# Optimization experiments

Measured on AMD Instinct MI355X. Metric: run time of the kernel, lower is better.

The kernel has to match this reference:

```python
import jax, jax.numpy as jnp
import numpy as np

BANDS, D_MODEL, NCLASS = 200, 256, 17
EXPAND, D_STATE, D_CONV, HEADDIM = 2, 128, 4, 64
D_INNER = EXPAND * D_MODEL            # 512
NHEADS = D_INNER // HEADDIM           # 8
D_IN_PROJ = 2 * D_INNER + 2 * D_STATE + NHEADS  # 1288 (ngroups=1)
CHUNK = 256


def _segsum(a):
    # a: (..., Q) -> (..., Q, Q); out[i,j] = sum_{k=j+1..i} a[k] (i>=j), else -inf
    q = a.shape[-1]
    cs = jnp.cumsum(a, axis=-1)
    d = cs[..., :, None] - cs[..., None, :]
    mask = jnp.tril(jnp.ones((q, q), dtype=bool))
    return jnp.where(mask, d, -jnp.inf)


def _ssd(Xd, Adt, B, C, Q):
    # Chunked SSD (exact selective-scan). Xd=(b,l,h,p) is x*dt, Adt=(b,l,h) is A*dt, B,C=(b,l,n)
    b, l, h, p = Xd.shape
    n = B.shape[-1]
    c = l // Q
    Xc = Xd.reshape(b, c, Q, h, p)
    Bc = B.reshape(b, c, Q, n)
    Cc = C.reshape(b, c, Q, n)
    Ac = Adt.reshape(b, c, Q, h).transpose(0, 3, 1, 2)      # (b,h,c,Q)
    Acs = jnp.cumsum(Ac, axis=-1)
    Lm = jnp.exp(_segsum(Ac))                                # (b,h,c,Q,Q) lower-tri decay
    Yd = jnp.einsum('bcqn,bckn,bhcqk,bckhp->bcqhp', Cc, Bc, Lm, Xc)
    decay_states = jnp.exp(Acs[..., -1:] - Acs)              # (b,h,c,Q)
    states = jnp.einsum('bcqn,bhcq,bcqhp->bchpn', Bc, decay_states, Xc)
    chunk_decay = jnp.exp(Acs[..., -1])                      # (b,h,c)
    def step(carry, inp):
        s, d = inp
        return carry * d[..., None, None] + s, carry
    _, prev = jax.lax.scan(step, jnp.zeros((b, h, p, n), Xd.dtype),
                           (states.transpose(1, 0, 2, 3, 4), chunk_decay.transpose(2, 0, 1)))
    prev = prev.transpose(1, 0, 2, 3, 4)                     # (b,c,h,p,n) state entering each chunk
    Yo = jnp.einsum('bcqn,bchpn,bhcq->bcqhp', Cc, prev, jnp.exp(Acs))
    return (Yd + Yo).reshape(b, l, h, p)


def setup_inputs() -> dict:
    ks = jax.random.split(jax.random.key(0), 8)
    b, l = 16, 1024
    dt0 = jnp.exp(jax.random.uniform(ks[1], (NHEADS,), minval=np.log(1e-3), maxval=np.log(0.1)))
    return {
        'x': jax.random.normal(ks[0], (b, l, BANDS), jnp.float32),
        'w_inp': jax.random.normal(ks[2], (BANDS, D_MODEL)) * 0.05,
        'b_inp': jnp.zeros((D_MODEL,)),
        'w_in': jax.random.normal(ks[3], (D_MODEL, D_IN_PROJ)) * 0.05,
        'conv_w': jax.random.normal(ks[4], (D_CONV, D_INNER + 2 * D_STATE)) * 0.2,
        'conv_b': jnp.zeros((D_INNER + 2 * D_STATE,)),
        'dt_bias': jnp.log(jnp.expm1(dt0)),                 # inverse softplus
        'A_log': jnp.log(jnp.arange(1, NHEADS + 1, dtype=jnp.float32)),
        'D': jnp.ones((NHEADS,)),
        'rms_w': jnp.ones((D_INNER,)),
        'w_out': jax.random.normal(ks[5], (D_INNER, D_MODEL)) * 0.04,
        'ln_g': jnp.ones((D_MODEL,)),
        'ln_b': jnp.zeros((D_MODEL,)),
        'w_cls': jax.random.normal(ks[6], (D_MODEL, NCLASS)) * 0.06,
        'b_cls': jnp.zeros((NCLASS,)),
    }


def reference(x, w_inp, b_inp, w_in, conv_w, conv_b, dt_bias, A_log, D,
              rms_w, w_out, ln_g, ln_b, w_cls, b_cls):
    b, l, _ = x.shape
    u = x @ w_inp + b_inp                                    # input_proj: (b,l,d_model)
    zxbcdt = u @ w_in                                        # (b,l,1288)
    z, xBC, dt = jnp.split(zxbcdt, [D_INNER, 2 * D_INNER + 2 * D_STATE], axis=-1)
    dt = jax.nn.softplus(dt + dt_bias)                       # (b,l,nheads)
    # causal depthwise conv1d + SiLU
    xBC = jax.lax.conv_general_dilated(
        xBC, conv_w[:, None, :], (1,), [(D_CONV - 1, 0)],
        dimension_numbers=('NWC', 'WIO', 'NWC'),
        feature_group_count=D_INNER + 2 * D_STATE) + conv_b
    xBC = jax.nn.silu(xBC)
    xh, B, C = jnp.split(xBC, [D_INNER, D_INNER + D_STATE], axis=-1)
    xh = xh.reshape(b, l, NHEADS, HEADDIM)
    A = -jnp.exp(A_log)                                      # (nheads,)
    y = _ssd(xh * dt[..., None], dt * A, B, C, CHUNK)        # (b,l,h,p)
    y = y + xh * D[None, None, :, None]                      # D skip
    y = y.reshape(b, l, D_INNER)
    # gated RMSNorm (norm_before_gate=False): rmsnorm(y * silu(z)) * w
    y = y * jax.nn.silu(z)
    y = y * jax.lax.rsqrt(jnp.mean(y * y, axis=-1, keepdims=True) + 1e-5) * rms_w
    y = y @ w_out                                            # out_proj (no bias)
    # classifier: LayerNorm -> Dropout(eval=identity) -> Linear
    mu = jnp.mean(y, axis=-1, keepdims=True)
    var = jnp.mean((y - mu) ** 2, axis=-1, keepdims=True)
    y = (y - mu) * jax.lax.rsqrt(var + 1e-5) * ln_g + ln_b
    return y @ w_cls + b_cls
```

## Files before the change

kernel.cpp:

```cpp
#include <hip/hip_runtime.h>
#include <math.h>

#define ROWS   16384L
#define LSEQ   1024
#define NB     16
#define DM     256
#define DPROJ  1288
#define XBCW   768
#define DIN    512
#define DSTATE 128
#define NH     8
#define HD     64
#define QLEN   256
#define NCHUNK 4
#define NCLS   17

typedef __attribute__((ext_vector_type(8))) short s16x8;
typedef __attribute__((ext_vector_type(4))) float f32x4;

#define GLOAD_LDS16(gsrc, ldst) \
  __builtin_amdgcn_global_load_lds((const __attribute__((address_space(1))) void*)(gsrc), \
      (__attribute__((address_space(3))) void*)(ldst), 16, 0, 0)

constexpr long O_GBF  = 0;
constexpr long O_ZX   = O_GBF + ROWS*DM;
constexpr long O_XBC  = O_ZX  + ROWS*DPROJ;
constexpr long O_DT   = O_XBC + ROWS*XBCW;
constexpr long O_ACS  = O_DT  + ROWS*NH;
constexpr long O_Y    = O_ACS + 131072;
constexpr long O_ST   = O_Y   + ROWS*DIN;
constexpr long O_Y2   = O_ST  + 4194304;
constexpr long O_XBF  = O_XBC;
constexpr long O_BBF  = O_XBC + 4200000;
constexpr long O_CBF  = O_XBC + 5300000;
constexpr long O_BT   = O_XBC + 6400000;
constexpr long O_YBF  = O_Y;
constexpr long O_XPBF = O_Y + 4300000;
constexpr long O_WCT  = O_Y + 6200000;
constexpr long O_WOUTT= O_Y + 6400000;
constexpr long O_WDT  = O_Y + 6500000;
constexpr long O_WCLST= O_Y + 6530000;
constexpr long O_WINT = O_Y + 6600000;
constexpr long O_WIPE = O_Y + 6800000;

__device__ inline unsigned short f2bf(float f) {
  union { float f; unsigned u; } v; v.f = f;
  unsigned r = v.u + 0x7FFFu + ((v.u >> 16) & 1u);
  return (unsigned short)(r >> 16);
}
__device__ inline float bf2f(unsigned short s) {
  union { unsigned u; float f; } v; v.u = ((unsigned)s) << 16; return v.f;
}

__global__ __launch_bounds__(256) void prep_misc(
    const float* __restrict__ x, unsigned short* __restrict__ xp,
    const float* __restrict__ w_in, unsigned short* __restrict__ w_inT,
    const float* __restrict__ wout, unsigned short* __restrict__ woutT,
    const float* __restrict__ w_inp, const float* __restrict__ b_inp,
    unsigned short* __restrict__ we,
    float* __restrict__ Wdt, float* __restrict__ bdt,
    const float* __restrict__ wcls, float* __restrict__ wclsT)
{
  int bid = blockIdx.x;
  int tid = threadIdx.x;
  if (bid < 3584) {
    long idx = (long)bid * 256 + tid;
    int q = (int)(idx % 56);
    long row = idx / 56;
    ushort4 o = {0, 0, 0, 0};
    if (q < 50) {
      float4 v = *(const float4*)&x[row * 200 + q * 4];
      o.x = f2bf(v.x); o.y = f2bf(v.y); o.z = f2bf(v.z); o.w = f2bf(v.w);
    } else if (q == 50) {
      o.x = 0x3F80;
    }
    *(ushort4*)&xp[row * 224 + q * 4] = o;
  } else if (bid < 4872) {
    long i = (long)(bid - 3584) * 256 + tid;
    int k = (int)(i & 255);
    long n = i >> 8;
    w_inT[i] = f2bf(w_in[(long)k * DPROJ + n]);
  } else if (bid < 5384) {
    long i = (long)(bid - 4872) * 256 + tid;
    int k = (int)(i & 511);
    long n = i >> 9;
    woutT[i] = f2bf(wout[(long)k * DM + n]);
  } else if (bid < 5608) {
    int i = (bid - 5384) * 256 + tid;
    int k = i >> 8, j = i & 255;
    float v = 0.f;
    if (k < 200)       v = w_inp[(long)k * 256 + j];
    else if (k == 200) v = b_inp[j];
    we[i] = f2bf(v);
  } else if (bid < 5659) {
    int k = (bid - 5608) * 4 + (tid >> 6);
    if (k > 200) return;
    int lane = tid & 63;
    int j0 = lane * 4;
    float4 xv = (k < 200) ? *(const float4*)&w_inp[(long)k * 256 + j0]
                          : *(const float4*)&b_inp[j0];
    float a0 = 0.f, a1 = 0.f, a2 = 0.f, a3 = 0.f, a4 = 0.f, a5 = 0.f, a6 = 0.f, a7 = 0.f;
    float xd[4] = {xv.x, xv.y, xv.z, xv.w};
#pragma unroll
    for (int d = 0; d < 4; ++d) {
      const float* wr = &w_in[(long)(j0 + d) * DPROJ + 1280];
      float4 wa = *(const float4*)wr;
      float4 wb = *(const float4*)(wr + 4);
      a0 = fmaf(xd[d], wa.x, a0); a1 = fmaf(xd[d], wa.y, a1);
      a2 = fmaf(xd[d], wa.z, a2); a3 = fmaf(xd[d], wa.w, a3);
      a4 = fmaf(xd[d], wb.x, a4); a5 = fmaf(xd[d], wb.y, a5);
      a6 = fmaf(xd[d], wb.z, a6); a7 = fmaf(xd[d], wb.w, a7);
    }
#pragma unroll
    for (int off = 32; off; off >>= 1) {
      a0 += __shfl_xor(a0, off); a1 += __shfl_xor(a1, off);
      a2 += __shfl_xor(a2, off); a3 += __shfl_xor(a3, off);
      a4 += __shfl_xor(a4, off); a5 += __shfl_xor(a5, off);
      a6 += __shfl_xor(a6, off); a7 += __shfl_xor(a7, off);
    }
    float o = a0;
    if (lane == 1) o = a1; if (lane == 2) o = a2; if (lane == 3) o = a3;
    if (lane == 4) o = a4; if (lane == 5) o = a5; if (lane == 6) o = a6;
    if (lane == 7) o = a7;
    if (lane < 8) {
      if (k < 200) Wdt[k * 8 + lane] = o;
      else         bdt[lane] = o;
    }
  } else {
    int i = (bid - 5659) * 256 + tid;
    if (i < NCLS * 256) {
      int j = i >> 8, k = i & 255;
      wclsT[i] = wcls[(long)k * NCLS + j];
    }
  }
}

__global__ __launch_bounds__(256) void gemm_bf16(
    const unsigned short* __restrict__ A, const unsigned short* __restrict__ BT,
    float* __restrict__ C, unsigned short* __restrict__ Cb,
    const float* __restrict__ bias, int M, int N, int K)
{
  __shared__ __align__(16) unsigned short As[128 * 32];
  __shared__ __align__(16) unsigned short Bs[128 * 32];
  const int tid = threadIdx.x;
  const int m0 = blockIdx.y * 128, n0 = blockIdx.x * 128;
  const int lane = tid & 63, wv = tid >> 6;
  const int wr = (wv >> 1) * 64, wc = (wv & 1) * 64;
  f32x4 acc[4][4];
#pragma unroll
  for (int i = 0; i < 4; ++i)
#pragma unroll
    for (int j = 0; j < 4; ++j) acc[i][j] = (f32x4){0.f, 0.f, 0.f, 0.f};

  for (int k0 = 0; k0 < K; k0 += 32) {
    __syncthreads();
#pragma unroll
    for (int s = 0; s < 2; ++s) {
      int idx = (tid + 256 * s) * 8;
      int r = idx >> 5, kk = idx & 31;
      GLOAD_LDS16(&A[(long)(m0 + r) * K + k0 + kk], &As[idx]);
    }
#pragma unroll
    for (int s = 0; s < 2; ++s) {
      int idx = (tid + 256 * s) * 8;
      int n = idx >> 5, kk = idx & 31;
      int srcn = (n0 + n < N) ? (n0 + n) : 0;
      GLOAD_LDS16(&BT[(long)srcn * K + k0 + kk], &Bs[idx]);
    }
    __syncthreads();
    s16x8 af[4], bf[4];
#pragma unroll
    for (int i = 0; i < 4; ++i)
      af[i] = *(const s16x8*)&As[(wr + i * 16 + (lane & 15)) * 32 + (lane >> 4) * 8];
#pragma unroll
    for (int j = 0; j < 4; ++j)
      bf[j] = *(const s16x8*)&Bs[(wc + j * 16 + (lane & 15)) * 32 + (lane >> 4) * 8];
#pragma unroll
    for (int i = 0; i < 4; ++i)
#pragma unroll
      for (int j = 0; j < 4; ++j)
        acc[i][j] = __builtin_amdgcn_mfma_f32_16x16x32_bf16(af[i], bf[j], acc[i][j], 0, 0, 0);
  }
  const int cr = (lane >> 4) * 4, cc = lane & 15;
#pragma unroll
  for (int i = 0; i < 4; ++i)
#pragma unroll
    for (int j = 0; j < 4; ++j) {
      int col = n0 + wc + j * 16 + cc;
      if (col < N) {
        long rowb = (long)(m0 + wr + i * 16 + cr);
        float bv = bias ? bias[col] : 0.f;
#pragma unroll
        for (int r = 0; r < 4; ++r) {
          float v = acc[i][j][r] + bv;
          if (C)  C[(rowb + r) * N + col] = v;
          if (Cb) Cb[(rowb + r) * (long)N + col] = f2bf(v);
        }
      }
    }
}

__global__ __launch_bounds__(256) void g_gemm_bf16(
    const unsigned short* __restrict__ Cbf, const unsigned short* __restrict__ Bbf,
    unsigned short* __restrict__ Gbf)
{
  int bc = blockIdx.z;
  unsigned short* Gout = Gbf + (long)bc * 65536;
  const int tid = threadIdx.x;
  const int m0 = blockIdx.y * 128, n0 = blockIdx.x * 128;
  if (blockIdx.x > blockIdx.y) {
    s16x8 z = {};
    for (int e = tid; e < 128 * 16; e += 256) {
      int r = e >> 4, seg = e & 15;
      *(s16x8*)&Gout[(long)(m0 + r) * 256 + n0 + seg * 8] = z;
    }
    return;
  }
  long rowbase = (long)(bc >> 2) * LSEQ + (bc & 3) * QLEN;
  const unsigned short* A  = Cbf + rowbase * 128;
  const unsigned short* BT = Bbf + rowbase * 128;
  __shared__ __align__(16) unsigned short As[128 * 32];
  __shared__ __align__(16) unsigned short Bs[128 * 32];
  const int lane = tid & 63, wv = tid >> 6;
  const int wr = (wv >> 1) * 64, wc = (wv & 1) * 64;
  f32x4 acc[4][4];
#pragma unroll
  for (int i = 0; i < 4; ++i)
#pragma unroll
    for (int j = 0; j < 4; ++j) acc[i][j] = (f32x4){0.f, 0.f, 0.f, 0.f};
  for (int k0 = 0; k0 < 128; k0 += 32) {
    __syncthreads();
#pragma unroll
    for (int s = 0; s < 2; ++s) {
      int idx = (tid + 256 * s) * 8;
      int r = idx >> 5, kk = idx & 31;
      GLOAD_LDS16(&A[(long)(m0 + r) * 128 + k0 + kk], &As[idx]);
      GLOAD_LDS16(&BT[(long)(n0 + r) * 128 + k0 + kk], &Bs[idx]);
    }
    __syncthreads();
    s16x8 af[4], bf[4];
#pragma unroll
    for (int i = 0; i < 4; ++i)
      af[i] = *(const s16x8*)&As[(wr + i * 16 + (lane & 15)) * 32 + (lane >> 4) * 8];
#pragma unroll
    for (int j = 0; j < 4; ++j)
      bf[j] = *(const s16x8*)&Bs[(wc + j * 16 + (lane & 15)) * 32 + (lane >> 4) * 8];
#pragma unroll
    for (int i = 0; i < 4; ++i)
#pragma unroll
      for (int j = 0; j < 4; ++j)
        acc[i][j] = __builtin_amdgcn_mfma_f32_16x16x32_bf16(af[i], bf[j], acc[i][j], 0, 0, 0);
  }
  const int cr = (lane >> 4) * 4, cc = lane & 15;
#pragma unroll
  for (int i = 0; i < 4; ++i)
#pragma unroll
    for (int j = 0; j < 4; ++j) {
      int col = n0 + wc + j * 16 + cc;
      int qb = m0 + wr + i * 16 + cr;
#pragma unroll
      for (int r = 0; r < 4; ++r)
        Gout[(long)(qb + r) * 256 + col] = (col <= qb + r) ? f2bf(acc[i][j][r]) : (unsigned short)0;
    }
}

__global__ __launch_bounds__(256) void conv_silu3(
    const unsigned short* __restrict__ zxb, const float* __restrict__ cw,
    const float* __restrict__ cb,
    unsigned short* __restrict__ Xbf, unsigned short* __restrict__ Bbf,
    unsigned short* __restrict__ Cbf)
{
  long idx = (long)blockIdx.x * 256 + threadIdx.x;
  if (idx >= ROWS * 192) return;
  int cq = (int)(idx % 192);
  long row = idx / 192;
  int t = (int)(row & 1023);
  int ch = cq * 4;
  float4 cbv = *(const float4*)&cb[ch];
  float a0 = cbv.x, a1 = cbv.y, a2 = cbv.z, a3 = cbv.w;
#pragma unroll
  for (int w = 0; w < 4; ++w) {
    int d = w - 3;
    if (t + d >= 0) {
      ushort4 zv = *(const ushort4*)&zxb[(row + d) * DPROJ + 512 + ch];
      float4 cwv = *(const float4*)&cw[w * XBCW + ch];
      a0 = fmaf(bf2f(zv.x), cwv.x, a0);
      a1 = fmaf(bf2f(zv.y), cwv.y, a1);
      a2 = fmaf(bf2f(zv.z), cwv.z, a2);
      a3 = fmaf(bf2f(zv.w), cwv.w, a3);
    }
  }
  ushort4 o;
  o.x = f2bf(a0 / (1.f + __expf(-a0)));
  o.y = f2bf(a1 / (1.f + __expf(-a1)));
  o.z = f2bf(a2 / (1.f + __expf(-a2)));
  o.w = f2bf(a3 / (1.f + __expf(-a3)));
  if (ch < 512)      *(ushort4*)&Xbf[row * DIN + ch] = o;
  else if (ch < 640) *(ushort4*)&Bbf[row * 128 + ch - 512] = o;
  else               *(ushort4*)&Cbf[row * 128 + ch - 640] = o;
}

__global__ __launch_bounds__(256) void dt_logits(
    const float* __restrict__ x, const float* __restrict__ Wdt,
    const float* __restrict__ bdt, const float* __restrict__ dtb,
    float* __restrict__ dtsp)
{
  __shared__ float xs[32][201];
  __shared__ float wdt_s[1600];
  long row0 = (long)blockIdx.x * 32;
  int tid = threadIdx.x;
#pragma unroll
  for (int s = 0; s < 25; ++s) {
    int e = tid + s * 256;
    int r = e / 200, c = e % 200;
    xs[r][c] = x[(row0 + r) * 200 + c];
  }
#pragma unroll
  for (int s = 0; s < 7; ++s) {
    int e = tid + s * 256;
    if (e < 1600) wdt_s[e] = Wdt[e];
  }
  __syncthreads();
  int r = tid >> 3, h = tid & 7;
  float acc = dtb[h] + bdt[h];
  for (int i = 0; i < 200; ++i)
    acc = fmaf(xs[r][i], wdt_s[i * 8 + h], acc);
  float sp = (acc > 20.f) ? acc : log1pf(__expf(acc));
  dtsp[(row0 + r) * NH + h] = sp;
}

__global__ __launch_bounds__(256) void dt_cumsum4(
    const float* __restrict__ dtsp, const float* __restrict__ alog,
    float* __restrict__ acs)
{
  int g = ((int)blockIdx.x * 256 + (int)threadIdx.x) >> 6;
  int lane = threadIdx.x & 63;
  int c = g & 3, h = (g >> 2) & 7, b = g >> 5;
  float Ah = -__expf(alog[h]);
  long rowbase = (long)b * LSEQ + c * QLEN;
  long abase = (((long)b * NH + h) * NCHUNK + c) * QLEN;
  float v[4];
#pragma unroll
  for (int j = 0; j < 4; ++j)
    v[j] = dtsp[(rowbase + lane * 4 + j) * NH + h] * Ah;
  v[1] += v[0]; v[2] += v[1]; v[3] += v[2];
  float tot = v[3];
  float run = tot;
#pragma unroll
  for (int d = 1; d < 64; d <<= 1) {
    float t = __shfl_up(run, d);
    if (lane >= d) run += t;
  }
  float excl = run - tot;
#pragma unroll
  for (int j = 0; j < 4; ++j) acs[abase + lane * 4 + j] = excl + v[j];
}

__global__ __launch_bounds__(256) void transB(const unsigned short* __restrict__ Bbf,
                                              unsigned short* __restrict__ BbfT)
{
  __shared__ unsigned short T[128][130];
  int bc = blockIdx.y, kh = blockIdx.x;
  int tid = threadIdx.x;
  long rowbase = (long)(bc >> 2) * LSEQ + (bc & 3) * QLEN + kh * 128;
  for (int e = tid; e < 128 * 128; e += 256) {
    int r = e >> 7, n = e & 127;
    T[r][n] = Bbf[(rowbase + r) * 128 + n];
  }
  __syncthreads();
  for (int e = tid; e < 128 * 128; e += 256) {
    int n = e >> 7, k = e & 127;
    BbfT[((long)bc * 128 + n) * 256 + kh * 128 + k] = T[k][n];
  }
}

__global__ __launch_bounds__(256) void yd_states7(
    const unsigned short* __restrict__ Xbf, const float* __restrict__ dtsp,
    const float* __restrict__ acs, const unsigned short* __restrict__ Gbf,
    const unsigned short* __restrict__ BbfT,
    unsigned short* __restrict__ ybf, unsigned short* __restrict__ st)
{
  int bid = blockIdx.x;
  int xcd = bid & 7, i0 = bid >> 3;
  int bc = xcd * 8 + (i0 >> 4);
  int rem = i0 & 15, h = rem >> 1, half = rem & 1;
  int c = bc & 3, b = bc >> 2;
  int bch = bc * 8 + h;

  __shared__ __align__(16) unsigned short XdT[64][264];
  __shared__ float AcsS[256], E1f[256], E2f[256], dts[256];

  const int tid = threadIdx.x;
  const int lane = tid & 63, wv = tid >> 6;
  const bool ydw = wv < 2;
  const int qb = half == 0 ? (wv == 0 ? 0 : 3) : (wv == 0 ? 1 : 2);
  const int q0 = qb * 64;
  const int n0w = half * 64 + (wv - 2) * 32;
  long rowbase = (long)b * LSEQ + c * QLEN;
  const unsigned short* Gb  = Gbf + (long)bc * 65536;
  const unsigned short* BTg = BbfT + (long)bc * 32768;

  AcsS[tid] = acs[(((long)b * NH + h) * NCHUNK + c) * QLEN + tid];
  dts[tid]  = dtsp[(rowbase + tid) * NH + h];
  __syncthreads();
  E1f[tid] = __expf(AcsS[tid] - AcsS[tid | 63]);
  E2f[tid] = __expf(AcsS[tid | 63] - AcsS[tid]);
  float rs_[4];
  rs_[0] = 1.f;
#pragma unroll
  for (int kt = 1; kt < 4; ++kt) rs_[kt] = __expf(AcsS[kt * 64 + 63] - AcsS[kt * 64 - 1]);
  __syncthreads();
  {
    int kb = wv * 64;
#pragma unroll
    for (int s = 0; s < 16; ++s) {
      int k4 = kb + s * 4;
      ushort4 pk;
      unsigned short* pp = (unsigned short*)&pk;
#pragma unroll
      for (int j = 0; j < 4; ++j) {
        int k = k4 + j;
        float v = bf2f(Xbf[(rowbase + k) * DIN + h * HD + lane]) * dts[k] * E2f[k];
        pp[j] = f2bf(v);
      }
      *(ushort4*)&XdT[lane][k4] = pk;
    }
  }
  __syncthreads();

  f32x4 accY[4][4], accS[4][2];
#pragma unroll
  for (int i = 0; i < 4; ++i)
#pragma unroll
    for (int j = 0; j < 4; ++j) accY[i][j] = (f32x4){0.f, 0.f, 0.f, 0.f};
#pragma unroll
  for (int i = 0; i < 4; ++i)
#pragma unroll
    for (int j = 0; j < 2; ++j) accS[i][j] = (f32x4){0.f, 0.f, 0.f, 0.f};

  for (int kt = 0; kt < 4; ++kt) {
    int qlo = kt * 64;
    if (ydw) {
      if (qb >= kt) {
        if (kt)
#pragma unroll
          for (int i = 0; i < 4; ++i)
#pragma unroll
            for (int j = 0; j < 4; ++j) accY[i][j] *= rs_[kt];
#pragma unroll
        for (int ks = 0; ks < 2; ++ks) {
          s16x8 bfr[4];
#pragma unroll
          for (int j = 0; j < 4; ++j)
            bfr[j] = *(const s16x8*)&XdT[j * 16 + (lane & 15)][qlo + ks * 32 + (lane >> 4) * 8];
#pragma unroll
          for (int i = 0; i < 4; ++i) {
            s16x8 a = *(const s16x8*)&Gb[(long)(q0 + i * 16 + (lane & 15)) * 256 + qlo + ks * 32 + (lane >> 4) * 8];
#pragma unroll
            for (int j = 0; j < 4; ++j)
              accY[i][j] = __builtin_amdgcn_mfma_f32_16x16x32_bf16(a, bfr[j], accY[i][j], 0, 0, 0);
          }
        }
      }
    } else {
      if (kt)
#pragma unroll
        for (int i = 0; i < 4; ++i)
#pragma unroll
          for (int j = 0; j < 2; ++j) accS[i][j] *= rs_[kt];
#pragma unroll
      for (int ks = 0; ks < 2; ++ks) {
        s16x8 afx[4];
#pragma unroll
        for (int i = 0; i < 4; ++i)
          afx[i] = *(const s16x8*)&XdT[i * 16 + (lane & 15)][qlo + ks * 32 + (lane >> 4) * 8];
#pragma unroll
        for (int j2 = 0; j2 < 2; ++j2) {
          s16x8 bt = *(const s16x8*)&BTg[(long)(n0w + j2 * 16 + (lane & 15)) * 256 + qlo + ks * 32 + (lane >> 4) * 8];
#pragma unroll
          for (int i = 0; i < 4; ++i)
            accS[i][j2] = __builtin_amdgcn_mfma_f32_16x16x32_bf16(afx[i], bt, accS[i][j2], 0, 0, 0);
        }
      }
    }
  }
  const int cr = (lane >> 4) * 4, cc = lane & 15;
  if (ydw) {
#pragma unroll
    for (int i = 0; i < 4; ++i)
#pragma unroll
      for (int j = 0; j < 4; ++j) {
        int q = q0 + i * 16 + cr;
        int p = j * 16 + cc;
#pragma unroll
        for (int r = 0; r < 4; ++r)
          ybf[(rowbase + q + r) * DIN + h * HD + p] = f2bf(accY[i][j][r] * E1f[q + r]);
      }
  } else {
#pragma unroll
    for (int i = 0; i < 4; ++i)
#pragma unroll
      for (int j2 = 0; j2 < 2; ++j2) {
        int p = i * 16 + cr;
        int n = n0w + j2 * 16 + cc;
#pragma unroll
        for (int r = 0; r < 4; ++r)
          st[(long)bch * 8192 + (long)(p + r) * 128 + n] = f2bf(accS[i][j2][r]);
      }
  }
}

__global__ void scan_states(unsigned short* __restrict__ st, const float* __restrict__ acs)
{
  long idx = (long)blockIdx.x * 256 + threadIdx.x;
  if (idx >= (long)NB * NH * 2048) return;
  long inner = idx & 2047;
  int h = (int)((idx >> 11) & 7);
  int b = (int)(idx >> 14);
  f32x4 carry = {0.f, 0.f, 0.f, 0.f};
  for (int c = 0; c < NCHUNK; ++c) {
    float dc = __expf(acs[(((long)b * NH + h) * NCHUNK + c) * QLEN + (QLEN - 1)]);
    long si = (((long)(b * NCHUNK + c) * NH + h) << 13) + inner * 4;
    ushort4 s4 = *(ushort4*)&st[si];
    f32x4 s = {bf2f(s4.x), bf2f(s4.y), bf2f(s4.z), bf2f(s4.w)};
    ushort4 o = {f2bf(carry[0]), f2bf(carry[1]), f2bf(carry[2]), f2bf(carry[3])};
    *(ushort4*)&st[si] = o;
    carry = carry * dc + s;
  }
}

__global__ __launch_bounds__(256) void yo_combine6(
    const unsigned short* __restrict__ Xbf, const unsigned short* __restrict__ Cbf,
    const unsigned short* __restrict__ prev, const float* __restrict__ acs,
    const float* __restrict__ Dp, unsigned short* __restrict__ ybf)
{
  int bid = blockIdx.x;
  int xcd = bid & 7, i0 = bid >> 3;
  int bc = xcd * 8 + (i0 >> 3), h = i0 & 7;
  int c = bc & 3, b = bc >> 2;
  int bch = bc * 8 + h;
  __shared__ float EqA[QLEN];
  const int tid = threadIdx.x;
  const int lane = tid & 63, wv = tid >> 6;
  long rowbase = (long)b * LSEQ + c * QLEN;
  EqA[tid] = __expf(acs[(((long)b * NH + h) * NCHUNK + c) * QLEN + tid]);
  __syncthreads();
  const unsigned short* Cb = Cbf + rowbase * 128;
  const unsigned short* pv = prev + (long)bch * 8192;
  f32x4 acc[4][4];
#pragma unroll
  for (int i = 0; i < 4; ++i)
#pragma unroll
    for (int j = 0; j < 4; ++j) acc[i][j] = (f32x4){0.f, 0.f, 0.f, 0.f};
#pragma unroll
  for (int ks = 0; ks < 4; ++ks) {
    int n0 = ks * 32 + (lane >> 4) * 8;
    s16x8 bf[4];
#pragma unroll
    for (int j = 0; j < 4; ++j) {
      int p = j * 16 + (lane & 15);
      bf[j] = *(const s16x8*)&pv[p * 128 + n0];
    }
#pragma unroll
    for (int i = 0; i < 4; ++i) {
      s16x8 af = *(const s16x8*)&Cb[(long)(wv * 64 + i * 16 + (lane & 15)) * 128 + n0];
#pragma unroll
      for (int j = 0; j < 4; ++j)
        acc[i][j] = __builtin_amdgcn_mfma_f32_16x16x32_bf16(af, bf[j], acc[i][j], 0, 0, 0);
    }
  }
  const int cr = (lane >> 4) * 4, cc = lane & 15;
  float Dh = Dp[h];
#pragma unroll
  for (int i = 0; i < 4; ++i)
#pragma unroll
    for (int j = 0; j < 4; ++j) {
      int q = wv * 64 + i * 16 + cr;
      int p = j * 16 + cc;
#pragma unroll
      for (int r = 0; r < 4; ++r) {
        long row = rowbase + q + r;
        long yi = row * DIN + h * HD + p;
        float xh = bf2f(Xbf[yi]);
        float pr = bf2f(ybf[yi]);
        ybf[yi] = f2bf(pr + acc[i][j][r] * EqA[q + r] + xh * Dh);
      }
    }
}

__global__ __launch_bounds__(256) void gated_rms3(
    unsigned short* __restrict__ ybf, const unsigned short* __restrict__ zxb,
    const float* __restrict__ rmsw)
{
  long row = blockIdx.x;
  int t = threadIdx.x;
  ushort2 yv = *(const ushort2*)&ybf[row * DIN + 2 * t];
  ushort2 zv = *(const ushort2*)&zxb[row * DPROJ + 2 * t];
  float z0 = bf2f(zv.x), z1 = bf2f(zv.y);
  float v0 = bf2f(yv.x) * (z0 / (1.f + __expf(-z0)));
  float v1 = bf2f(yv.y) * (z1 / (1.f + __expf(-z1)));
  float ss = v0 * v0 + v1 * v1;
#pragma unroll
  for (int off = 32; off; off >>= 1) ss += __shfl_down(ss, off);
  __shared__ float red[4];
  if ((t & 63) == 0) red[t >> 6] = ss;
  __syncthreads();
  float tot = red[0] + red[1] + red[2] + red[3];
  float scale = rsqrtf(tot * (1.f / DIN) + 1e-5f);
  ushort2 o;
  o.x = f2bf(v0 * scale * rmsw[2 * t]);
  o.y = f2bf(v1 * scale * rmsw[2 * t + 1]);
  *(ushort2*)&ybf[row * DIN + 2 * t] = o;
}

__global__ __launch_bounds__(256) void ln_cls2(
    const unsigned short* __restrict__ y2b, const float* __restrict__ g,
    const float* __restrict__ bb, const float* __restrict__ wclsT,
    const float* __restrict__ bcls, float* __restrict__ out)
{
  long row = (long)blockIdx.x * 4 + (threadIdx.x >> 6);
  int lane = threadIdx.x & 63;
  ushort4 yv = *(const ushort4*)&y2b[row * DM + lane * 4];
  float v0 = bf2f(yv.x), v1 = bf2f(yv.y), v2 = bf2f(yv.z), v3 = bf2f(yv.w);
  float s = v0 + v1 + v2 + v3;
  float q = v0 * v0 + v1 * v1 + v2 * v2 + v3 * v3;
#pragma unroll
  for (int off = 32; off; off >>= 1) {
    s += __shfl_xor(s, off);
    q += __shfl_xor(q, off);
  }
  float mu = s * (1.f / DM);
  float rstd = rsqrtf(q * (1.f / DM) - mu * mu + 1e-5f);
  float4 gv = *(const float4*)&g[lane * 4];
  float4 bv = *(const float4*)&bb[lane * 4];
  float y0 = (v0 - mu) * rstd * gv.x + bv.x;
  float y1 = (v1 - mu) * rstd * gv.y + bv.y;
  float y2_ = (v2 - mu) * rstd * gv.z + bv.z;
  float y3 = (v3 - mu) * rstd * gv.w + bv.w;
  float accs[NCLS];
#pragma unroll
  for (int j = 0; j < NCLS; ++j) {
    float4 wv = *(const float4*)&wclsT[j * 256 + lane * 4];
    accs[j] = y0 * wv.x + y1 * wv.y + y2_ * wv.z + y3 * wv.w;
  }
#pragma unroll
  for (int off = 32; off; off >>= 1)
#pragma unroll
    for (int j = 0; j < NCLS; ++j) accs[j] += __shfl_xor(accs[j], off);
  float o = accs[0] + bcls[0];
#pragma unroll
  for (int j = 1; j < NCLS; ++j)
    if (lane == j) o = accs[j] + bcls[j];
  if (lane < NCLS) out[row * NCLS + lane] = o;
}

extern "C" void kernel_launch(void* const* d_in, const int* in_sizes, int n_in,
                              void* d_out, int out_size, void* d_ws, size_t ws_size,
                              hipStream_t stream)
{
  const float* x     = (const float*)d_in[0];
  const float* w_inp = (const float*)d_in[1];
  const float* b_inp = (const float*)d_in[2];
  const float* w_in  = (const float*)d_in[3];
  const float* convw = (const float*)d_in[4];
  const float* convb = (const float*)d_in[5];
  const float* dtb   = (const float*)d_in[6];
  const float* alog  = (const float*)d_in[7];
  const float* Dp    = (const float*)d_in[8];
  const float* rmsw  = (const float*)d_in[9];
  const float* wout  = (const float*)d_in[10];
  const float* lng   = (const float*)d_in[11];
  const float* lnb   = (const float*)d_in[12];
  const float* wcls  = (const float*)d_in[13];
  const float* bcls  = (const float*)d_in[14];
  float* out = (float*)d_out;
  float* ws  = (float*)d_ws;

  float* dtsp = ws + O_DT;
  float* acs  = ws + O_ACS;
  float* Wdt  = ws + O_WDT;
  float* bdt  = Wdt + 1600;
  float* wclsT= ws + O_WCLST;
  unsigned short* Gbf    = (unsigned short*)(ws + O_GBF);
  unsigned short* zxb    = (unsigned short*)(ws + O_ZX);
  unsigned short* Xbf    = (unsigned short*)(ws + O_XBF);
  unsigned short* Bbf    = (unsigned short*)(ws + O_BBF);
  unsigned short* Cbf    = (unsigned short*)(ws + O_CBF);
  unsigned short* BbfT   = (unsigned short*)(ws + O_BT);
  unsigned short* ybf    = (unsigned short*)(ws + O_YBF);
  unsigned short* xp_bf  = (unsigned short*)(ws + O_XPBF);
  unsigned short* WcombT = (unsigned short*)(ws + O_WCT);
  unsigned short* woutT  = (unsigned short*)(ws + O_WOUTT);
  unsigned short* w_inT  = (unsigned short*)(ws + O_WINT);
  unsigned short* we_bf  = (unsigned short*)(ws + O_WIPE);
  unsigned short* st     = (unsigned short*)(ws + O_ST);
  unsigned short* y2b    = (unsigned short*)(ws + O_Y2);

  prep_misc<<<5676, 256, 0, stream>>>(x, xp_bf, w_in, w_inT, wout, woutT,
                                      w_inp, b_inp, we_bf, Wdt, bdt, wcls, wclsT);
  gemm_bf16<<<dim3(2, 11), 256, 0, stream>>>(w_inT, we_bf, nullptr, WcombT, nullptr, 1408, 224, 256);
  gemm_bf16<<<dim3(11, 128), 256, 0, stream>>>(xp_bf, WcombT, nullptr, zxb, nullptr, 16384, DPROJ, 224);
  conv_silu3<<<12288, 256, 0, stream>>>(zxb, convw, convb, Xbf, Bbf, Cbf);
  dt_logits<<<512, 256, 0, stream>>>(x, Wdt, bdt, dtb, dtsp);
  dt_cumsum4<<<128, 256, 0, stream>>>(dtsp, alog, acs);
  transB<<<dim3(2, 64), 256, 0, stream>>>(Bbf, BbfT);
  g_gemm_bf16<<<dim3(2, 2, 64), 256, 0, stream>>>(Cbf, Bbf, Gbf);
  yd_states7<<<1024, 256, 0, stream>>>(Xbf, dtsp, acs, Gbf, BbfT, ybf, st);
  scan_states<<<1024, 256, 0, stream>>>(st, acs);
  yo_combine6<<<512, 256, 0, stream>>>(Xbf, Cbf, st, acs, Dp, ybf);
  gated_rms3<<<16384, 256, 0, stream>>>(ybf, zxb, rmsw);
  gemm_bf16<<<dim3(2, 128), 256, 0, stream>>>(ybf, woutT, nullptr, y2b, nullptr, 16384, DM, DIN);
  ln_cls2<<<4096, 256, 0, stream>>>(y2b, lng, lnb, wclsT, bcls, out);
}
```

Measured before the change: 209.4 us.

## Trim in-proj width, fuse transpose with G gemm, vectorize conv and RMS kernels

After: 190.4 us. -9.1%, faster.

```diff
diff --git a/kernel.cpp b/kernel.cpp
--- a/kernel.cpp
+++ b/kernel.cpp
@@ -6,6 +6,7 @@
 #define NB     16
 #define DM     256
 #define DPROJ  1288
+#define ZXW    1280
 #define XBCW   768
 #define DIN    512
 #define DSTATE 128
@@ -16,6 +17,7 @@
 #define NCLS   17
 
 typedef __attribute__((ext_vector_type(8))) short s16x8;
+typedef __attribute__((ext_vector_type(8))) unsigned short u16x8;
 typedef __attribute__((ext_vector_type(4))) float f32x4;
 
 #define GLOAD_LDS16(gsrc, ldst) \
@@ -50,6 +52,16 @@
 }
 __device__ inline float bf2f(unsigned short s) {
   union { unsigned u; float f; } v; v.u = ((unsigned)s) << 16; return v.f;
+}
+
+__device__ inline void xcd_swizzle(int gx, int& bx, int& by) {
+  int nwg = gx * (int)gridDim.y;
+  int lid = (int)blockIdx.y * gx + (int)blockIdx.x;
+  int q = nwg >> 3, r = nwg & 7;
+  int xcd = lid & 7, idx = lid >> 3;
+  int base = xcd < r ? xcd * (q + 1) : r * (q + 1) + (xcd - r) * q;
+  int w = base + idx;
+  bx = w % gx; by = w / gx;
 }
 
 __global__ __launch_bounds__(256) void prep_misc(
@@ -140,10 +152,12 @@
     float* __restrict__ C, unsigned short* __restrict__ Cb,
     const float* __restrict__ bias, int M, int N, int K)
 {
+  int bx, by;
+  xcd_swizzle(gridDim.x, bx, by);
   __shared__ __align__(16) unsigned short As[128 * 32];
   __shared__ __align__(16) unsigned short Bs[128 * 32];
   const int tid = threadIdx.x;
-  const int m0 = blockIdx.y * 128, n0 = blockIdx.x * 128;
+  const int m0 = by * 128, n0 = bx * 128;
   const int lane = tid & 63, wv = tid >> 6;
   const int wr = (wv >> 1) * 64, wc = (wv & 1) * 64;
   f32x4 acc[4][4];
@@ -200,22 +214,42 @@
     }
 }
 
-__global__ __launch_bounds__(256) void g_gemm_bf16(
-    const unsigned short* __restrict__ Cbf, const unsigned short* __restrict__ Bbf,
-    unsigned short* __restrict__ Gbf)
-{
-  int bc = blockIdx.z;
-  unsigned short* Gout = Gbf + (long)bc * 65536;
+__global__ __launch_bounds__(256) void trans_g(
+    const unsigned short* __restrict__ Bbf, unsigned short* __restrict__ BbfT,
+    const unsigned short* __restrict__ Cbf, unsigned short* __restrict__ Gbf)
+{
+  const int bid = blockIdx.x;
   const int tid = threadIdx.x;
-  const int m0 = blockIdx.y * 128, n0 = blockIdx.x * 128;
-  if (blockIdx.x > blockIdx.y) {
+  if (bid < 128) {
+    __shared__ unsigned short T[128][130];
+    int bc = bid >> 1, kh = bid & 1;
+    long rowbase = (long)(bc >> 2) * LSEQ + (bc & 3) * QLEN + kh * 128;
+    for (int e = tid; e < 128 * 128; e += 256) {
+      int r = e >> 7, n = e & 127;
+      T[r][n] = Bbf[(rowbase + r) * 128 + n];
+    }
+    __syncthreads();
+    for (int e = tid; e < 128 * 128; e += 256) {
+      int n = e >> 7, k = e & 127;
+      BbfT[((long)bc * 128 + n) * 256 + kh * 128 + k] = T[k][n];
+    }
+    return;
+  }
+  if (bid >= 320) {
+    int bc = bid - 320;
+    unsigned short* Gout = Gbf + (long)bc * 65536;
     s16x8 z = {};
     for (int e = tid; e < 128 * 16; e += 256) {
       int r = e >> 4, seg = e & 15;
-      *(s16x8*)&Gout[(long)(m0 + r) * 256 + n0 + seg * 8] = z;
+      *(s16x8*)&Gout[(long)r * 256 + 128 + seg * 8] = z;
     }
     return;
   }
+  int bid2 = bid - 128;
+  int t = bid2 % 3, bc = bid2 / 3;
+  int m0 = (t == 0) ? 0 : 128;
+  int n0 = (t == 2) ? 128 : 0;
+  unsigned short* Gout = Gbf + (long)bc * 65536;
   long rowbase = (long)(bc >> 2) * LSEQ + (bc & 3) * QLEN;
   const unsigned short* A  = Cbf + rowbase * 128;
   const unsigned short* BT = Bbf + rowbase * 128;
@@ -264,40 +298,49 @@
     }
 }
 
-__global__ __launch_bounds__(256) void conv_silu3(
+__global__ __launch_bounds__(256) void conv_silu4(
     const unsigned short* __restrict__ zxb, const float* __restrict__ cw,
     const float* __restrict__ cb,
     unsigned short* __restrict__ Xbf, unsigned short* __restrict__ Bbf,
     unsigned short* __restrict__ Cbf)
 {
   long idx = (long)blockIdx.x * 256 + threadIdx.x;
-  if (idx >= ROWS * 192) return;
-  int cq = (int)(idx % 192);
-  long row = idx / 192;
+  if (idx >= ROWS * 96) return;
+  int co = (int)(idx % 96);
+  long row = idx / 96;
   int t = (int)(row & 1023);
-  int ch = cq * 4;
-  float4 cbv = *(const float4*)&cb[ch];
-  float a0 = cbv.x, a1 = cbv.y, a2 = cbv.z, a3 = cbv.w;
+  int ch = co * 8;
+  float a[8];
+  {
+    float4 cb0 = *(const float4*)&cb[ch];
+    float4 cb1 = *(const float4*)&cb[ch + 4];
+    a[0] = cb0.x; a[1] = cb0.y; a[2] = cb0.z; a[3] = cb0.w;
+    a[4] = cb1.x; a[5] = cb1.y; a[6] = cb1.z; a[7] = cb1.w;
+  }
 #pragma unroll
   for (int w = 0; w < 4; ++w) {
     int d = w - 3;
     if (t + d >= 0) {
-      ushort4 zv = *(const ushort4*)&zxb[(row + d) * DPROJ + 512 + ch];
-      float4 cwv = *(const float4*)&cw[w * XBCW + ch];
-      a0 = fmaf(bf2f(zv.x), cwv.x, a0);
-      a1 = fmaf(bf2f(zv.y), cwv.y, a1);
-      a2 = fmaf(bf2f(zv.z), cwv.z, a2);
-      a3 = fmaf(bf2f(zv.w), cwv.w, a3);
-    }
-  }
-  ushort4 o;
-  o.x = f2bf(a0 / (1.f + __expf(-a0)));
-  o.y = f2bf(a1 / (1.f + __expf(-a1)));
-  o.z = f2bf(a2 / (1.f + __expf(-a2)));
-  o.w = f2bf(a3 / (1.f + __expf(-a3)));
-  if (ch < 512)      *(ushort4*)&Xbf[row * DIN + ch] = o;
-  else if (ch < 640) *(ushort4*)&Bbf[row * 128 + ch - 512] = o;
-  else               *(ushort4*)&Cbf[row * 128 + ch - 640] = o;
+      u16x8 zv = *(const u16x8*)&zxb[(row + d) * ZXW + 512 + ch];
+      float4 cw0 = *(const float4*)&cw[w * XBCW + ch];
+      float4 cw1 = *(const float4*)&cw[w * XBCW + ch + 4];
+      a[0] = fmaf(bf2f(zv[0]), cw0.x, a[0]);
+      a[1] = fmaf(bf2f(zv[1]), cw0.y, a[1]);
+      a[2] = fmaf(bf2f(zv[2]), cw0.z, a[2]);
+      a[3] = fmaf(bf2f(zv[3]), cw0.w, a[3]);
+      a[4] = fmaf(bf2f(zv[4]), cw1.x, a[4]);
+      a[5] = fmaf(bf2f(zv[5]), cw1.y, a[5]);
+      a[6] = fmaf(bf2f(zv[6]), cw1.z, a[6]);
+      a[7] = fmaf(bf2f(zv[7]), cw1.w, a[7]);
+    }
+  }
+  u16x8 o;
+#pragma unroll
+  for (int i = 0; i < 8; ++i)
+    o[i] = f2bf(a[i] / (1.f + __expf(-a[i])));
+  if (ch < 512)      *(u16x8*)&Xbf[row * DIN + ch] = o;
+  else if (ch < 640) *(u16x8*)&Bbf[row * 128 + ch - 512] = o;
+  else               *(u16x8*)&Cbf[row * 128 + ch - 640] = o;
 }
 
 __global__ __launch_bounds__(256) void dt_logits(
@@ -354,24 +397,6 @@
   float excl = run - tot;
 #pragma unroll
   for (int j = 0; j < 4; ++j) acs[abase + lane * 4 + j] = excl + v[j];
-}
-
-__global__ __launch_bounds__(256) void transB(const unsigned short* __restrict__ Bbf,
-                                              unsigned short* __restrict__ BbfT)
-{
-  __shared__ unsigned short T[128][130];
-  int bc = blockIdx.y, kh = blockIdx.x;
-  int tid = threadIdx.x;
-  long rowbase = (long)(bc >> 2) * LSEQ + (bc & 3) * QLEN + kh * 128;
-  for (int e = tid; e < 128 * 128; e += 256) {
-    int r = e >> 7, n = e & 127;
-    T[r][n] = Bbf[(rowbase + r) * 128 + n];
-  }
-  __syncthreads();
-  for (int e = tid; e < 128 * 128; e += 256) {
-    int n = e >> 7, k = e & 127;
-    BbfT[((long)bc * 128 + n) * 256 + kh * 128 + k] = T[k][n];
-  }
 }
 
 __global__ __launch_bounds__(256) void yd_states7(
@@ -588,29 +613,32 @@
     }
 }
 
-__global__ __launch_bounds__(256) void gated_rms3(
+__global__ __launch_bounds__(256) void gated_rms4(
     unsigned short* __restrict__ ybf, const unsigned short* __restrict__ zxb,
     const float* __restrict__ rmsw)
 {
-  long row = blockIdx.x;
-  int t = threadIdx.x;
-  ushort2 yv = *(const ushort2*)&ybf[row * DIN + 2 * t];
-  ushort2 zv = *(const ushort2*)&zxb[row * DPROJ + 2 * t];
-  float z0 = bf2f(zv.x), z1 = bf2f(zv.y);
-  float v0 = bf2f(yv.x) * (z0 / (1.f + __expf(-z0)));
-  float v1 = bf2f(yv.y) * (z1 / (1.f + __expf(-z1)));
-  float ss = v0 * v0 + v1 * v1;
-#pragma unroll
-  for (int off = 32; off; off >>= 1) ss += __shfl_down(ss, off);
-  __shared__ float red[4];
-  if ((t & 63) == 0) red[t >> 6] = ss;
-  __syncthreads();
-  float tot = red[0] + red[1] + red[2] + red[3];
-  float scale = rsqrtf(tot * (1.f / DIN) + 1e-5f);
-  ushort2 o;
-  o.x = f2bf(v0 * scale * rmsw[2 * t]);
-  o.y = f2bf(v1 * scale * rmsw[2 * t + 1]);
-  *(ushort2*)&ybf[row * DIN + 2 * t] = o;
+  long row = (long)blockIdx.x * 4 + (threadIdx.x >> 6);
+  int lane = threadIdx.x & 63;
+  u16x8 yv = *(const u16x8*)&ybf[row * DIN + lane * 8];
+  u16x8 zv = *(const u16x8*)&zxb[row * ZXW + lane * 8];
+  float v[8];
+  float ss = 0.f;
+#pragma unroll
+  for (int i = 0; i < 8; ++i) {
+    float z = bf2f(zv[i]);
+    v[i] = bf2f(yv[i]) * (z / (1.f + __expf(-z)));
+    ss = fmaf(v[i], v[i], ss);
+  }
+#pragma unroll
+  for (int off = 32; off; off >>= 1) ss += __shfl_xor(ss, off);
+  float scale = rsqrtf(ss * (1.f / DIN) + 1e-5f);
+  u16x8 o;
+#pragma unroll
+  for (int i = 0; i < 8; ++i) {
+    float w = rmsw[lane * 8 + i];
+    o[i] = f2bf(v[i] * scale * w);
+  }
+  *(u16x8*)&ybf[row * DIN + lane * 8] = o;
 }
 
 __global__ __launch_bounds__(256) void ln_cls2(
@@ -699,16 +727,15 @@
   prep_misc<<<5676, 256, 0, stream>>>(x, xp_bf, w_in, w_inT, wout, woutT,
                                       w_inp, b_inp, we_bf, Wdt, bdt, wcls, wclsT);
   gemm_bf16<<<dim3(2, 11), 256, 0, stream>>>(w_inT, we_bf, nullptr, WcombT, nullptr, 1408, 224, 256);
-  gemm_bf16<<<dim3(11, 128), 256, 0, stream>>>(xp_bf, WcombT, nullptr, zxb, nullptr, 16384, DPROJ, 224);
-  conv_silu3<<<12288, 256, 0, stream>>>(zxb, convw, convb, Xbf, Bbf, Cbf);
+  gemm_bf16<<<dim3(10, 128), 256, 0, stream>>>(xp_bf, WcombT, nullptr, zxb, nullptr, 16384, ZXW, 224);
+  conv_silu4<<<6144, 256, 0, stream>>>(zxb, convw, convb, Xbf, Bbf, Cbf);
   dt_logits<<<512, 256, 0, stream>>>(x, Wdt, bdt, dtb, dtsp);
   dt_cumsum4<<<128, 256, 0, stream>>>(dtsp, alog, acs);
-  transB<<<dim3(2, 64), 256, 0, stream>>>(Bbf, BbfT);
-  g_gemm_bf16<<<dim3(2, 2, 64), 256, 0, stream>>>(Cbf, Bbf, Gbf);
+  trans_g<<<384, 256, 0, stream>>>(Bbf, BbfT, Cbf, Gbf);
   yd_states7<<<1024, 256, 0, stream>>>(Xbf, dtsp, acs, Gbf, BbfT, ybf, st);
   scan_states<<<1024, 256, 0, stream>>>(st, acs);
   yo_combine6<<<512, 256, 0, stream>>>(Xbf, Cbf, st, acs, Dp, ybf);
-  gated_rms3<<<16384, 256, 0, stream>>>(ybf, zxb, rmsw);
+  gated_rms4<<<4096, 256, 0, stream>>>(ybf, zxb, rmsw);
   gemm_bf16<<<dim3(2, 128), 256, 0, stream>>>(ybf, woutT, nullptr, y2b, nullptr, 16384, DM, DIN);
   ln_cls2<<<4096, 256, 0, stream>>>(y2b, lng, lnb, wclsT, bcls, out);
 }
```
